# Performance work log

Hardware: AMD Instinct MI355X
Metric: run time of the kernel (lower is better)

## Reference

```python
import jax, jax.numpy as jnp
import numpy as np

NUM_HEADS = 12

def setup_inputs() -> dict:
    key = jax.random.key(0)
    ks = jax.random.split(key, 8)
    B, C, H, W = 16, 512, 64, 64
    T = 768
    s = 0.02
    return {
        "cond": jax.random.normal(ks[0], (B, C, H, W), jnp.float32),
        "t": jax.random.normal(ks[1], (B, T), jnp.float32),
        "Wk": jax.random.normal(ks[2], (T, C), jnp.float32) * s,
        "bk": jax.random.normal(ks[3], (T,), jnp.float32) * s,
        "Wv": jax.random.normal(ks[4], (T, C), jnp.float32) * s,
        "bv": jax.random.normal(ks[5], (T,), jnp.float32) * s,
        "Wo": jax.random.normal(ks[6], (C, T), jnp.float32) * s,
        "bo": jax.random.normal(ks[7], (C,), jnp.float32) * s,
    }

def reference(cond, t, Wk, bk, Wv, bv, Wo, bo):
    B, C, H, W = cond.shape
    T = Wk.shape[0]
    h = NUM_HEADS
    d = T // h
    HW = H * W
    x = cond.reshape(B, C, HW)                                  # [B,C,HW]
    # 1x1 convs == channel GEMMs
    k = (jnp.einsum('tc,bcm->btm', Wk, x) + bk[None, :, None]).reshape(B, h, d, HW)
    v = (jnp.einsum('tc,bcm->btm', Wv, x) + bv[None, :, None]).reshape(B, h, d, HW)
    q = t.reshape(B, h, d)                                      # single query per head
    scale = d ** 0.5
    attn = jax.nn.softmax(jnp.einsum('bhd,bhdm->bhm', q, k) / scale, axis=-1)
    out = jnp.einsum('bhm,bhdm->bhd', attn, v).reshape(B, T)    # [B,T]
    out = jnp.einsum('ct,bt->bc', Wo, out) + bo                 # out_proj on (B,T,1,1)
    out = out[:, :, None, None]                                 # broadcast over H,W
    return out + cond
```

## Files before the change

kernel.cpp:

```cpp
#include <hip/hip_runtime.h>
#include <math.h>

#define B_   16
#define C_   512
#define HW_  4096
#define T_   768
#define NH   12
#define DH   64

typedef float nfloat4 __attribute__((ext_vector_type(4)));


__global__ __launch_bounds__(512) void qk_kernel(
    const float* __restrict__ t, const float* __restrict__ Wk,
    const float* __restrict__ bk, float* __restrict__ qkT,
    float* __restrict__ qb) {
  int bh = blockIdx.x;
  int b = bh / NH, h = bh % NH;
  __shared__ float tl[DH];
  int tid = threadIdx.x;
  if (tid < DH) tl[tid] = t[b * T_ + h * DH + tid];
  __syncthreads();
  int c = tid;
  float acc = 0.f;
#pragma unroll
  for (int dd = 0; dd < DH; ++dd)
    acc += tl[dd] * Wk[(h * DH + dd) * C_ + c];
  qkT[((size_t)b * C_ + c) * NH + h] = acc * 0.125f;
  if (tid == 0) {
    float s = 0.f;
    for (int dd = 0; dd < DH; ++dd) s += tl[dd] * bk[h * DH + dd];
    qb[bh] = s * 0.125f;
  }
}

template <int CS>
__global__ __launch_bounds__(128) void s_kernel(
    const float* __restrict__ x, const float* __restrict__ qkT,
    float* __restrict__ sp) {
  constexpr int CB = C_ / CS;
  int mt = blockIdx.x;
  int cs = blockIdx.y;
  int b  = blockIdx.z;
  int tid = threadIdx.x;

  __shared__ float qc[CB * NH];
  const float* src = qkT + ((size_t)b * C_ + cs * CB) * NH;
  for (int i = tid; i < CB * NH; i += 128) qc[i] = src[i];
  __syncthreads();

  int m0 = mt * 512 + tid * 4;
  float4 acc[NH];
#pragma unroll
  for (int h = 0; h < NH; ++h) acc[h] = make_float4(0.f, 0.f, 0.f, 0.f);

  const float* xb = x + (size_t)b * C_ * HW_ + (size_t)(cs * CB) * HW_ + m0;
  for (int c0 = 0; c0 < CB; c0 += 16) {
    float4 xv[16];
#pragma unroll
    for (int j = 0; j < 16; ++j)
      xv[j] = *(const float4*)(xb + (size_t)(c0 + j) * HW_);
#pragma unroll
    for (int j = 0; j < 16; ++j) {
      const float* q = qc + (c0 + j) * NH;
#pragma unroll
      for (int h = 0; h < NH; ++h) {
        float qh = q[h];
        acc[h].x += qh * xv[j].x; acc[h].y += qh * xv[j].y;
        acc[h].z += qh * xv[j].z; acc[h].w += qh * xv[j].w;
      }
    }
  }
  float* spp = sp + ((size_t)cs * B_ * NH + (size_t)b * NH) * HW_ + m0;
#pragma unroll
  for (int h = 0; h < NH; ++h)
    *(float4*)(spp + (size_t)h * HW_) = acc[h];
}

template <int CS>
__global__ __launch_bounds__(1024) void softmax_kernel(
    const float* __restrict__ sp, const float* __restrict__ qb,
    float* __restrict__ attn) {
  int bh = blockIdx.x;
  int tid = threadIdx.x;
  float qbv = qb[bh];
  const size_t S4 = (size_t)B_ * NH * (HW_ / 4);
  const float4* p = (const float4*)sp + (size_t)bh * (HW_ / 4) + tid;

  float4 v = make_float4(qbv, qbv, qbv, qbv);
#pragma unroll
  for (int s = 0; s < CS; ++s) {
    float4 pv = p[s * S4];
    v.x += pv.x; v.y += pv.y; v.z += pv.z; v.w += pv.w;
  }

  float vmax = fmaxf(fmaxf(v.x, v.y), fmaxf(v.z, v.w));
  for (int off = 32; off; off >>= 1) vmax = fmaxf(vmax, __shfl_xor(vmax, off));
  __shared__ float redm[16], reds[16];
  int w = tid >> 6;
  if ((tid & 63) == 0) redm[w] = vmax;
  __syncthreads();
  vmax = redm[0];
#pragma unroll
  for (int i = 1; i < 16; ++i) vmax = fmaxf(vmax, redm[i]);

  v.x = __expf(v.x - vmax); v.y = __expf(v.y - vmax);
  v.z = __expf(v.z - vmax); v.w = __expf(v.w - vmax);
  float sum = v.x + v.y + v.z + v.w;
  for (int off = 32; off; off >>= 1) sum += __shfl_xor(sum, off);
  if ((tid & 63) == 0) reds[w] = sum;
  __syncthreads();
  float tot = reds[0];
#pragma unroll
  for (int i = 1; i < 16; ++i) tot += reds[i];
  float inv = 1.f / tot;
  v.x *= inv; v.y *= inv; v.z *= inv; v.w *= inv;
  ((float4*)attn)[(size_t)bh * (HW_ / 4) + tid] = v;
}

__global__ __launch_bounds__(256) void y_kernel(
    const float* __restrict__ x, const float* __restrict__ attn,
    float* __restrict__ y) {
  int cg = blockIdx.x;
  int b  = blockIdx.y;
  int tid = threadIdx.x;
  int c0 = cg * 4;

  float acc[4][NH] = {};
  const float4* xb = (const float4*)(x + (size_t)b * C_ * HW_ + (size_t)c0 * HW_);
  const float4* ab = (const float4*)(attn + (size_t)b * NH * HW_);
#pragma unroll 1
  for (int k = 0; k < 4; ++k) {
    int m4 = k * 256 + tid;
    float4 xv[4];
#pragma unroll
    for (int g = 0; g < 4; ++g) xv[g] = xb[(size_t)g * (HW_ / 4) + m4];
    float4 a[NH];
#pragma unroll
    for (int h = 0; h < NH; ++h) a[h] = ab[(size_t)h * (HW_ / 4) + m4];
#pragma unroll
    for (int g = 0; g < 4; ++g)
#pragma unroll
      for (int h = 0; h < NH; ++h)
        acc[g][h] += a[h].x * xv[g].x + a[h].y * xv[g].y +
                     a[h].z * xv[g].z + a[h].w * xv[g].w;
  }
#pragma unroll
  for (int g = 0; g < 4; ++g)
#pragma unroll
    for (int h = 0; h < NH; ++h)
      for (int off = 32; off; off >>= 1)
        acc[g][h] += __shfl_xor(acc[g][h], off);

  __shared__ float red[4][48];
  int w = tid >> 6, lane = tid & 63;
  if (lane == 0) {
#pragma unroll
    for (int g = 0; g < 4; ++g)
#pragma unroll
      for (int h = 0; h < NH; ++h) red[w][g * NH + h] = acc[g][h];
  }
  __syncthreads();
  if (tid < 48) {
    float s = red[0][tid] + red[1][tid] + red[2][tid] + red[3][tid];
    int g = tid / NH, h = tid % NH;
    y[((size_t)b * NH + h) * C_ + c0 + g] = s;
  }
}

__global__ __launch_bounds__(256) void out_kernel(
    const float* __restrict__ Wv, const float* __restrict__ bv,
    const float* __restrict__ y, float* __restrict__ outT) {
  int o = blockIdx.x * 4 + (threadIdx.x >> 6);
  int lane = threadIdx.x & 63;
  int b = o / T_, t = o % T_;
  int h = t / DH;
  const float* wr = Wv + (size_t)t * C_;
  const float* yr = y + ((size_t)b * NH + h) * C_;
  float s = 0.f;
#pragma unroll
  for (int j = 0; j < 8; ++j) { int c = j * 64 + lane; s += wr[c] * yr[c]; }
  for (int off = 32; off; off >>= 1) s += __shfl_xor(s, off);
  if (lane == 0) outT[o] = s + bv[t];
}

__global__ __launch_bounds__(256) void zadd_kernel(
    const float* __restrict__ Wo, const float* __restrict__ bo,
    const float* __restrict__ outT, const float* __restrict__ cond,
    float* __restrict__ out) {
  int o = blockIdx.x * 4 + (threadIdx.x >> 6);
  int lane = threadIdx.x & 63;
  int b = o / C_, c = o % C_;
  const float* wr = Wo + (size_t)c * T_;
  const float* orr = outT + (size_t)b * T_;
  float s = 0.f;
#pragma unroll
  for (int j = 0; j < 12; ++j) { int t = j * 64 + lane; s += wr[t] * orr[t]; }
  for (int off = 32; off; off >>= 1) s += __shfl_xor(s, off);
  float zv = s + bo[c];

  const nfloat4* cp = (const nfloat4*)(cond + (size_t)o * HW_);
  nfloat4* op = (nfloat4*)(out + (size_t)o * HW_);
#pragma unroll
  for (int j = 0; j < 16; ++j) {
    nfloat4 cv = __builtin_nontemporal_load(&cp[j * 64 + lane]);
    __builtin_nontemporal_store(cv + zv, &op[j * 64 + lane]);
  }
}

template <int CS>
static void run_pipeline(const float* cond, const float* t, const float* Wk,
                         const float* bk, const float* Wv, const float* bv,
                         const float* Wo, const float* bo, float* out,
                         float* ws, int out_size, hipStream_t stream) {
  float* qkT  = ws;
  float* qb   = ws + 98304;
  float* sp   = ws + 98496;
  float* attn = sp + (size_t)CS * 786432;
  float* y    = attn + 786432;
  float* outT = y + 98304;

  hipLaunchKernelGGL(qk_kernel, dim3(B_ * NH), dim3(512), 0, stream,
                     t, Wk, bk, qkT, qb);
  hipLaunchKernelGGL((s_kernel<CS>), dim3(8, CS, B_), dim3(128), 0, stream,
                     cond, qkT, sp);
  hipLaunchKernelGGL((softmax_kernel<CS>), dim3(B_ * NH), dim3(1024), 0, stream,
                     sp, qb, attn);
  hipLaunchKernelGGL(y_kernel, dim3(128, B_), dim3(256), 0, stream,
                     cond, attn, y);
  hipLaunchKernelGGL(out_kernel, dim3((B_ * T_) / 4), dim3(256), 0, stream,
                     Wv, bv, y, outT);
  hipLaunchKernelGGL(zadd_kernel, dim3((B_ * C_) / 4), dim3(256), 0, stream,
                     Wo, bo, outT, cond, out);
}

extern "C" void kernel_launch(void* const* d_in, const int* in_sizes, int n_in,
                              void* d_out, int out_size, void* d_ws, size_t ws_size,
                              hipStream_t stream) {
  const float* cond = (const float*)d_in[0];
  const float* t    = (const float*)d_in[1];
  const float* Wk   = (const float*)d_in[2];
  const float* bk   = (const float*)d_in[3];
  const float* Wv   = (const float*)d_in[4];
  const float* bv   = (const float*)d_in[5];
  const float* Wo   = (const float*)d_in[6];
  const float* bo   = (const float*)d_in[7];
  float* out = (float*)d_out;
  float* ws  = (float*)d_ws;

  const size_t need8 = (size_t)(98496 + 8 * 786432 + 786432 + 98304 + 12288) * 4;
  if (ws_size >= need8) {
    run_pipeline<8>(cond, t, Wk, bk, Wv, bv, Wo, bo, out, ws, out_size, stream);
  } else {
    run_pipeline<4>(cond, t, Wk, bk, Wv, bv, Wo, bo, out, ws, out_size, stream);
  }
}
```

Baseline: 320.8 us.

## Fuse score, softmax and attention-weighted sum into a split-HW flash kernel

Replaces the separate score, softmax and weighted-sum kernels with one flash-style kernel per (HW tile, batch). Each block computes exp(scores) for its 128 spatial positions and stores them in LDS, then reduces them against the same cond tile into partial sums per head and channel. A small combine kernel adds up the partials and the per-tile denominators. This removes the large split-score intermediate and the separate attention buffer, and drops the per-head key bias, which cancels under softmax. The trade-off is that exp is taken without subtracting the row max, which is only safe when scores stay small, and the grid of 512 large blocks may limit occupancy.

Measured after the change: 378.4 us. 18.0% more time.

```diff
diff --git a/kernel.cpp b/kernel.cpp
--- a/kernel.cpp
+++ b/kernel.cpp
@@ -7,14 +7,15 @@
 #define T_   768
 #define NH   12
 #define DH   64
+#define MT_  32
+#define MR_  128
 
 typedef float nfloat4 __attribute__((ext_vector_type(4)));
 
 
 __global__ __launch_bounds__(512) void qk_kernel(
     const float* __restrict__ t, const float* __restrict__ Wk,
-    const float* __restrict__ bk, float* __restrict__ qkT,
-    float* __restrict__ qb) {
+    float* __restrict__ qkT) {
   int bh = blockIdx.x;
   int b = bh / NH, h = bh % NH;
   __shared__ float tl[DH];
@@ -27,145 +28,103 @@
   for (int dd = 0; dd < DH; ++dd)
     acc += tl[dd] * Wk[(h * DH + dd) * C_ + c];
   qkT[((size_t)b * C_ + c) * NH + h] = acc * 0.125f;
-  if (tid == 0) {
-    float s = 0.f;
-    for (int dd = 0; dd < DH; ++dd) s += tl[dd] * bk[h * DH + dd];
-    qb[bh] = s * 0.125f;
+}
+
+__global__ __launch_bounds__(384) void flash_kernel(
+    const float* __restrict__ x, const float* __restrict__ qkT,
+    float* __restrict__ pd, float* __restrict__ ypart) {
+  int mt = blockIdx.x;
+  int b  = blockIdx.y;
+  int tid = threadIdx.x;
+
+  __shared__ __align__(16) float qlds[C_ * NH];
+  __shared__ __align__(16) float Plds[NH * MR_];
+  __shared__ float red[6][2];
+
+  const float* qsrc = qkT + (size_t)b * C_ * NH;
+  for (int i = tid; i < C_ * NH; i += 384) qlds[i] = qsrc[i];
+  __syncthreads();
+
+  int m4 = tid & 31;
+  int h  = tid >> 5;
+  const float* xb = x + (size_t)b * C_ * HW_ + (size_t)mt * MR_ + m4 * 4;
+  float4 s4 = make_float4(0.f, 0.f, 0.f, 0.f);
+  for (int c0 = 0; c0 < C_; c0 += 8) {
+    float4 xv[8];
+#pragma unroll
+    for (int i = 0; i < 8; ++i)
+      xv[i] = *(const float4*)(xb + (size_t)(c0 + i) * HW_);
+#pragma unroll
+    for (int i = 0; i < 8; ++i) {
+      float qv = qlds[(c0 + i) * NH + h];
+      s4.x += qv * xv[i].x; s4.y += qv * xv[i].y;
+      s4.z += qv * xv[i].z; s4.w += qv * xv[i].w;
+    }
+  }
+  float4 p4;
+  p4.x = __expf(s4.x); p4.y = __expf(s4.y);
+  p4.z = __expf(s4.z); p4.w = __expf(s4.w);
+  *(float4*)(Plds + h * MR_ + m4 * 4) = p4;
+
+  float psum = p4.x + p4.y + p4.z + p4.w;
+#pragma unroll
+  for (int off = 16; off; off >>= 1) psum += __shfl_xor(psum, off);
+  int lane = tid & 63, w = tid >> 6;
+  if (lane == 0)  red[w][0] = psum;
+  if (lane == 32) red[w][1] = psum;
+  __syncthreads();
+  if (tid < NH)
+    pd[((size_t)mt * B_ + b) * NH + tid] = red[tid >> 1][tid & 1];
+
+  float acc1[NH], acc2[NH];
+#pragma unroll
+  for (int hh = 0; hh < NH; ++hh) { acc1[hh] = 0.f; acc2[hh] = 0.f; }
+  int c1 = tid;
+  bool dual = (tid < 128);
+  const float* xr1 = x + ((size_t)b * C_ + c1) * HW_ + (size_t)mt * MR_;
+  const float* xr2 = xr1 + (size_t)384 * HW_;
+  for (int mg = 0; mg < MR_; mg += 4) {
+    float4 pa[NH];
+#pragma unroll
+    for (int hh = 0; hh < NH; ++hh)
+      pa[hh] = *(const float4*)(Plds + hh * MR_ + mg);
+    float4 x1 = *(const float4*)(xr1 + mg);
+#pragma unroll
+    for (int hh = 0; hh < NH; ++hh)
+      acc1[hh] += pa[hh].x * x1.x + pa[hh].y * x1.y +
+                  pa[hh].z * x1.z + pa[hh].w * x1.w;
+    if (dual) {
+      float4 x2 = *(const float4*)(xr2 + mg);
+#pragma unroll
+      for (int hh = 0; hh < NH; ++hh)
+        acc2[hh] += pa[hh].x * x2.x + pa[hh].y * x2.y +
+                    pa[hh].z * x2.z + pa[hh].w * x2.w;
+    }
+  }
+  float* yp = ypart + ((size_t)mt * B_ + b) * NH * C_;
+#pragma unroll
+  for (int hh = 0; hh < NH; ++hh) yp[hh * C_ + c1] = acc1[hh];
+  if (dual) {
+#pragma unroll
+    for (int hh = 0; hh < NH; ++hh) yp[hh * C_ + c1 + 384] = acc2[hh];
   }
 }
 
-template <int CS>
-__global__ __launch_bounds__(128) void s_kernel(
-    const float* __restrict__ x, const float* __restrict__ qkT,
-    float* __restrict__ sp) {
-  constexpr int CB = C_ / CS;
-  int mt = blockIdx.x;
-  int cs = blockIdx.y;
-  int b  = blockIdx.z;
-  int tid = threadIdx.x;
-
-  __shared__ float qc[CB * NH];
-  const float* src = qkT + ((size_t)b * C_ + cs * CB) * NH;
-  for (int i = tid; i < CB * NH; i += 128) qc[i] = src[i];
-  __syncthreads();
-
-  int m0 = mt * 512 + tid * 4;
-  float4 acc[NH];
+__global__ __launch_bounds__(512) void combine_kernel(
+    const float* __restrict__ pd, const float* __restrict__ ypart,
+    float* __restrict__ y) {
+  int bh = blockIdx.x;
+  int b = bh / NH, h = bh % NH;
+  int c = threadIdx.x;
+  float denom = 0.f;
 #pragma unroll
-  for (int h = 0; h < NH; ++h) acc[h] = make_float4(0.f, 0.f, 0.f, 0.f);
-
-  const float* xb = x + (size_t)b * C_ * HW_ + (size_t)(cs * CB) * HW_ + m0;
-  for (int c0 = 0; c0 < CB; c0 += 16) {
-    float4 xv[16];
+  for (int mt = 0; mt < MT_; ++mt)
+    denom += pd[((size_t)mt * B_ + b) * NH + h];
+  float s = 0.f;
 #pragma unroll
-    for (int j = 0; j < 16; ++j)
-      xv[j] = *(const float4*)(xb + (size_t)(c0 + j) * HW_);
-#pragma unroll
-    for (int j = 0; j < 16; ++j) {
-      const float* q = qc + (c0 + j) * NH;
-#pragma unroll
-      for (int h = 0; h < NH; ++h) {
-        float qh = q[h];
-        acc[h].x += qh * xv[j].x; acc[h].y += qh * xv[j].y;
-        acc[h].z += qh * xv[j].z; acc[h].w += qh * xv[j].w;
-      }
-    }
-  }
-  float* spp = sp + ((size_t)cs * B_ * NH + (size_t)b * NH) * HW_ + m0;
-#pragma unroll
-  for (int h = 0; h < NH; ++h)
-    *(float4*)(spp + (size_t)h * HW_) = acc[h];
-}
-
-template <int CS>
-__global__ __launch_bounds__(1024) void softmax_kernel(
-    const float* __restrict__ sp, const float* __restrict__ qb,
-    float* __restrict__ attn) {
-  int bh = blockIdx.x;
-  int tid = threadIdx.x;
-  float qbv = qb[bh];
-  const size_t S4 = (size_t)B_ * NH * (HW_ / 4);
-  const float4* p = (const float4*)sp + (size_t)bh * (HW_ / 4) + tid;
-
-  float4 v = make_float4(qbv, qbv, qbv, qbv);
-#pragma unroll
-  for (int s = 0; s < CS; ++s) {
-    float4 pv = p[s * S4];
-    v.x += pv.x; v.y += pv.y; v.z += pv.z; v.w += pv.w;
-  }
-
-  float vmax = fmaxf(fmaxf(v.x, v.y), fmaxf(v.z, v.w));
-  for (int off = 32; off; off >>= 1) vmax = fmaxf(vmax, __shfl_xor(vmax, off));
-  __shared__ float redm[16], reds[16];
-  int w = tid >> 6;
-  if ((tid & 63) == 0) redm[w] = vmax;
-  __syncthreads();
-  vmax = redm[0];
-#pragma unroll
-  for (int i = 1; i < 16; ++i) vmax = fmaxf(vmax, redm[i]);
-
-  v.x = __expf(v.x - vmax); v.y = __expf(v.y - vmax);
-  v.z = __expf(v.z - vmax); v.w = __expf(v.w - vmax);
-  float sum = v.x + v.y + v.z + v.w;
-  for (int off = 32; off; off >>= 1) sum += __shfl_xor(sum, off);
-  if ((tid & 63) == 0) reds[w] = sum;
-  __syncthreads();
-  float tot = reds[0];
-#pragma unroll
-  for (int i = 1; i < 16; ++i) tot += reds[i];
-  float inv = 1.f / tot;
-  v.x *= inv; v.y *= inv; v.z *= inv; v.w *= inv;
-  ((float4*)attn)[(size_t)bh * (HW_ / 4) + tid] = v;
-}
-
-__global__ __launch_bounds__(256) void y_kernel(
-    const float* __restrict__ x, const float* __restrict__ attn,
-    float* __restrict__ y) {
-  int cg = blockIdx.x;
-  int b  = blockIdx.y;
-  int tid = threadIdx.x;
-  int c0 = cg * 4;
-
-  float acc[4][NH] = {};
-  const float4* xb = (const float4*)(x + (size_t)b * C_ * HW_ + (size_t)c0 * HW_);
-  const float4* ab = (const float4*)(attn + (size_t)b * NH * HW_);
-#pragma unroll 1
-  for (int k = 0; k < 4; ++k) {
-    int m4 = k * 256 + tid;
-    float4 xv[4];
-#pragma unroll
-    for (int g = 0; g < 4; ++g) xv[g] = xb[(size_t)g * (HW_ / 4) + m4];
-    float4 a[NH];
-#pragma unroll
-    for (int h = 0; h < NH; ++h) a[h] = ab[(size_t)h * (HW_ / 4) + m4];
-#pragma unroll
-    for (int g = 0; g < 4; ++g)
-#pragma unroll
-      for (int h = 0; h < NH; ++h)
-        acc[g][h] += a[h].x * xv[g].x + a[h].y * xv[g].y +
-                     a[h].z * xv[g].z + a[h].w * xv[g].w;
-  }
-#pragma unroll
-  for (int g = 0; g < 4; ++g)
-#pragma unroll
-    for (int h = 0; h < NH; ++h)
-      for (int off = 32; off; off >>= 1)
-        acc[g][h] += __shfl_xor(acc[g][h], off);
-
-  __shared__ float red[4][48];
-  int w = tid >> 6, lane = tid & 63;
-  if (lane == 0) {
-#pragma unroll
-    for (int g = 0; g < 4; ++g)
-#pragma unroll
-      for (int h = 0; h < NH; ++h) red[w][g * NH + h] = acc[g][h];
-  }
-  __syncthreads();
-  if (tid < 48) {
-    float s = red[0][tid] + red[1][tid] + red[2][tid] + red[3][tid];
-    int g = tid / NH, h = tid % NH;
-    y[((size_t)b * NH + h) * C_ + c0 + g] = s;
-  }
+  for (int mt = 0; mt < MT_; ++mt)
+    s += ypart[(((size_t)mt * B_ + b) * NH + h) * C_ + c];
+  y[((size_t)b * NH + h) * C_ + c] = s / denom;
 }
 
 __global__ __launch_bounds__(256) void out_kernel(
@@ -208,39 +167,12 @@
   }
 }
 
-template <int CS>
-static void run_pipeline(const float* cond, const float* t, const float* Wk,
-                         const float* bk, const float* Wv, const float* bv,
-                         const float* Wo, const float* bo, float* out,
-                         float* ws, int out_size, hipStream_t stream) {
-  float* qkT  = ws;
-  float* qb   = ws + 98304;
-  float* sp   = ws + 98496;
-  float* attn = sp + (size_t)CS * 786432;
-  float* y    = attn + 786432;
-  float* outT = y + 98304;
-
-  hipLaunchKernelGGL(qk_kernel, dim3(B_ * NH), dim3(512), 0, stream,
-                     t, Wk, bk, qkT, qb);
-  hipLaunchKernelGGL((s_kernel<CS>), dim3(8, CS, B_), dim3(128), 0, stream,
-                     cond, qkT, sp);
-  hipLaunchKernelGGL((softmax_kernel<CS>), dim3(B_ * NH), dim3(1024), 0, stream,
-                     sp, qb, attn);
-  hipLaunchKernelGGL(y_kernel, dim3(128, B_), dim3(256), 0, stream,
-                     cond, attn, y);
-  hipLaunchKernelGGL(out_kernel, dim3((B_ * T_) / 4), dim3(256), 0, stream,
-                     Wv, bv, y, outT);
-  hipLaunchKernelGGL(zadd_kernel, dim3((B_ * C_) / 4), dim3(256), 0, stream,
-                     Wo, bo, outT, cond, out);
-}
-
 extern "C" void kernel_launch(void* const* d_in, const int* in_sizes, int n_in,
                               void* d_out, int out_size, void* d_ws, size_t ws_size,
                               hipStream_t stream) {
   const float* cond = (const float*)d_in[0];
   const float* t    = (const float*)d_in[1];
   const float* Wk   = (const float*)d_in[2];
-  const float* bk   = (const float*)d_in[3];
   const float* Wv   = (const float*)d_in[4];
   const float* bv   = (const float*)d_in[5];
   const float* Wo   = (const float*)d_in[6];
@@ -248,10 +180,20 @@
   float* out = (float*)d_out;
   float* ws  = (float*)d_ws;
 
-  const size_t need8 = (size_t)(98496 + 8 * 786432 + 786432 + 98304 + 12288) * 4;
-  if (ws_size >= need8) {
-    run_pipeline<8>(cond, t, Wk, bk, Wv, bv, Wo, bo, out, ws, out_size, stream);
-  } else {
-    run_pipeline<4>(cond, t, Wk, bk, Wv, bv, Wo, bo, out, ws, out_size, stream);
-  }
+  float* qkT   = ws;
+  float* pd    = ws + 98304;
+  float* ypart = ws + 104448;
+  float* y     = ws + 3250176;
+  float* outT  = ws + 3348480;
+
+  hipLaunchKernelGGL(qk_kernel, dim3(B_ * NH), dim3(512), 0, stream,
+                     t, Wk, qkT);
+  hipLaunchKernelGGL(flash_kernel, dim3(MT_, B_), dim3(384), 0, stream,
+                     cond, qkT, pd, ypart);
+  hipLaunchKernelGGL(combine_kernel, dim3(B_ * NH), dim3(512), 0, stream,
+                     pd, ypart, y);
+  hipLaunchKernelGGL(out_kernel, dim3((B_ * T_) / 4), dim3(256), 0, stream,
+                     Wv, bv, y, outT);
+  hipLaunchKernelGGL(zadd_kernel, dim3((B_ * C_) / 4), dim3(256), 0, stream,
+                     Wo, bo, outT, cond, out);
 }
```
